# Kernel optimization log

Hardware: AMD Instinct MI355X
Metric: run time of the kernel (lower is better)

## Reference

```python
import jax, jax.numpy as jnp
import numpy as np

N_S, N_T, E = 50000, 50000, 600000
D_IN, D_H, D_OUT = 256, 128, 64


def setup_inputs() -> dict:
    key = jax.random.key(0)
    k1, k2, k3, k4, k5, k6 = jax.random.split(key, 6)
    edge_src = jax.random.randint(k1, (E,), 0, N_S, dtype=jnp.int32)
    edge_dst = jax.random.randint(k2, (E,), 0, N_T, dtype=jnp.int32)
    edge_index = jnp.stack([edge_src, edge_dst], axis=0)  # [2, E]
    x_s = jax.random.normal(k3, (N_S, D_IN), dtype=jnp.float32)
    x_t = jax.random.normal(k4, (N_T, D_IN), dtype=jnp.float32)
    W0 = jax.random.normal(k5, (D_IN, D_H), dtype=jnp.float32) * (1.0 / np.sqrt(D_IN))
    W1 = jax.random.normal(k6, (D_H, D_OUT), dtype=jnp.float32) * (1.0 / np.sqrt(D_H))
    return {"edge_index": edge_index, "x_s": x_s, "x_t": x_t, "W0": W0, "W1": W1}


def gcn_conv(x, src, dst, W):
    """PyG GCNConv, bias=False: D^{-1/2}(A+I)D^{-1/2} (x @ W)."""
    N = x.shape[0]
    h = x @ W  # [N, out]
    loops = jnp.arange(N, dtype=src.dtype)
    s = jnp.concatenate([src, loops])  # add self-loops
    d = jnp.concatenate([dst, loops])
    deg = jax.ops.segment_sum(jnp.ones_like(d, dtype=h.dtype), d, num_segments=N)
    dinv = jnp.where(deg > 0, jax.lax.rsqrt(deg), 0.0)
    norm = dinv[s] * dinv[d]  # [E+N]
    return jax.ops.segment_sum(h[s] * norm[:, None], d, num_segments=N)


def reference(edge_index, x_s, x_t, W0, W1):
    n_s = x_s.shape[0]
    src = edge_index[0]
    dst = edge_index[1] + n_s  # targets live in the x_t block
    acts = [jax.nn.relu, lambda v: v]
    Ws = [W0, W1]
    for W, act in zip(Ws, acts):
        x = jnp.concatenate([x_s, x_t], axis=0)
        x = act(gcn_conv(x, src, dst, W))
        x_s, x_t = x[:n_s], x[n_s:]
    return (x_s, x_t)
```

## Files before the change

### kernel.cpp

```cpp
#include <hip/hip_runtime.h>
#include <cstdint>
#include <cstddef>

typedef unsigned short u16;
typedef unsigned int   u32;
typedef __attribute__((ext_vector_type(8))) short bf16x8;
typedef __attribute__((ext_vector_type(4))) float f32x4;

#define D_IN  256
#define D_H   128
#define D_OUT 64

__device__ __forceinline__ float bf2f(u16 u){
  union { u32 i; float f; } v; v.i = ((u32)u) << 16; return v.f;
}
__device__ __forceinline__ u16 f2bf(float f){
  union { float f; u32 i; } v; v.f = f;
  u32 r = (v.i + 0x7fffu + ((v.i >> 16) & 1u)) >> 16;
  return (u16)r;
}

__global__ void k_wprep(const float* __restrict__ W0, const float* __restrict__ W1,
                        u16* __restrict__ W0t, u16* __restrict__ W1t,
                        int* __restrict__ deg, int n_t){
  int i = blockIdx.x * 256 + threadIdx.x;
  if (i < 128 * 256){
    int n = i >> 8, k = i & 255;
    W0t[i] = f2bf(W0[(size_t)k * 128 + n]);
  } else if (i < 128 * 256 + 64 * 128){
    int j = i - 128 * 256;
    int n = j >> 7, k = j & 127;
    W1t[j] = f2bf(W1[(size_t)k * 64 + n]);
  } else if (i - (128 * 256 + 64 * 128) < n_t){
    deg[i - (128 * 256 + 64 * 128)] = 0;
  }
}

__global__ __launch_bounds__(256) void k_off(const int* __restrict__ deg, int N,
                                             int* __restrict__ off, int* __restrict__ cursor,
                                             float* __restrict__ dinv){
  __shared__ int s[256];
  __shared__ int sbase[256];
  const int tid = threadIdx.x;
  const int bid = blockIdx.x;
  const int i   = bid * 256 + tid;
  int acc = 0;
  const int lim = bid * 256;
  for (int j = tid; j < lim; j += 256) acc += deg[j];
  sbase[tid] = acc;
  int v = (i < N) ? deg[i] : 0;
  s[tid] = v;
  __syncthreads();
  for (int o = 128; o > 0; o >>= 1){
    if (tid < o) sbase[tid] += sbase[tid + o];
    __syncthreads();
  }
  for (int o = 1; o < 256; o <<= 1){
    int tv = (tid >= o) ? s[tid - o] : 0;
    __syncthreads();
    s[tid] += tv;
    __syncthreads();
  }
  if (i < N){
    int excl = s[tid] - v + sbase[0];
    off[i] = excl;
    cursor[i] = excl;
    dinv[i] = rsqrtf((float)v + 1.0f);
  }
}

__global__ void k_fill(const int* __restrict__ src, const int* __restrict__ dst,
                       int E, int* __restrict__ cursor, int* __restrict__ csr){
  int e = blockIdx.x * 256 + threadIdx.x;
  if (e < E){
    int d = dst[e];
    int p = atomicAdd(&cursor[d], 1);
    csr[p] = src[e];
  }
}

__global__ __launch_bounds__(512, 4) void k_g1(
    const float* __restrict__ Xs, const float* __restrict__ Xt,
    const u16* __restrict__ W0t, int M, int n_s,
    const int* __restrict__ dst, int E, int* __restrict__ deg, int nbDeg,
    u16* __restrict__ out)
{
  __shared__ u16 Bs[128 * 256];
  const int t = threadIdx.x;

  if ((int)blockIdx.x < nbDeg){
    const int stride = nbDeg * 512;
    for (int e = blockIdx.x * 512 + t; e < E; e += stride)
      atomicAdd(&deg[dst[e]], 1);
    return;
  }

  const int wave = t >> 6, lane = t & 63;
  const int lm   = lane & 15, quad = lane >> 4;
  const int gw   = ((int)blockIdx.x - nbDeg) * 8 + wave;
  const int row  = gw * 16 + lm;

  int cr = (row < M) ? row : 0;
  const float* pa = ((cr < n_s) ? (Xs + (size_t)cr * D_IN)
                                : (Xt + (size_t)(cr - n_s) * D_IN)) + quad * 8;

  float4 a[8][2];
  a[0][0] = *(const float4*)(pa +  0); a[0][1] = *(const float4*)(pa +  4);
  a[1][0] = *(const float4*)(pa + 32); a[1][1] = *(const float4*)(pa + 36);

  {
    const int n = t >> 2;
    const int c = t & 3;
    const u16* wsrc = W0t + (size_t)n * 256 + c * 64;
    char* brow = (char*)Bs + n * 512;
    const int sw = (n & 15) << 4;
    #pragma unroll
    for (int j = 0; j < 8; j++){
      int off = (c * 128 + j * 16) ^ sw;
      *(int4*)(brow + off) = *(const int4*)(wsrc + j * 8);
    }
  }

  #pragma unroll
  for (int s = 2; s < 8; s++){
    a[s][0] = *(const float4*)(pa + s * 32);
    a[s][1] = *(const float4*)(pa + s * 32 + 4);
  }
  __builtin_amdgcn_sched_barrier(0);

  f32x4 acc[8];
  const f32x4 z = {0.f, 0.f, 0.f, 0.f};
  #pragma unroll
  for (int nf = 0; nf < 8; nf++) acc[nf] = z;

  __syncthreads();

  const char* bb = (const char*)Bs + lm * 512;
  const int lmx = lm << 4;

  #pragma unroll
  for (int kk = 0; kk < 8; kk++){
    bf16x8 af;
    {
      const float* fa = (const float*)&a[kk][0];
      u16 tmp[8];
      #pragma unroll
      for (int q = 0; q < 8; q++) tmp[q] = f2bf(fa[q]);
      af = *(const bf16x8*)tmp;
    }
    const int koff = (kk * 64 + quad * 16) ^ lmx;
    #pragma unroll
    for (int nf = 0; nf < 8; nf++){
      bf16x8 bf = *(const bf16x8*)(bb + nf * 8192 + koff);
      acc[nf] = __builtin_amdgcn_mfma_f32_16x16x32_bf16(af, bf, acc[nf], 0, 0, 0);
    }
  }

  __syncthreads();
  u16* wreg = Bs + wave * 2048;
  #pragma unroll
  for (int nf = 0; nf < 8; nf++){
    #pragma unroll
    for (int rr = 0; rr < 4; rr++){
      int rl = quad * 4 + rr;
      int c  = nf * 16 + lm;
      wreg[rl * 128 + (c ^ (quad << 5))] = f2bf(acc[nf][rr]);
    }
  }
  {
    const int g = lane >> 4, l = lane & 15;
    const int wrow0 = gw * 16;
    #pragma unroll
    for (int i = 0; i < 4; i++){
      int rl = i * 4 + g;
      int m  = wrow0 + rl;
      bf16x8 v = *(const bf16x8*)&wreg[rl * 128 + ((l ^ (i << 2)) << 3)];
      if (m < M) *(bf16x8*)(out + (size_t)m * D_H + l * 8) = v;
    }
  }
}

__device__ __forceinline__ void aggf_body(
    const int* __restrict__ off, const int* __restrict__ deg,
    const int* __restrict__ csr, const float* __restrict__ dinv,
    u16* __restrict__ h1, int n_s, int n_t, int w, int lane)
{
  if (w >= n_t) return;
  const int g = lane >> 4;
  const int c = lane & 15;
  int start = off[w];
  int n     = deg[w];

  float r[8], p[8];
  #pragma unroll
  for (int q = 0; q < 8; q++){ r[q] = 0.f; p[q] = 0.f; }

  int i = 0;
  for (; i + 8 <= n; i += 8){
    int sa = csr[start + i + g];
    int sb = csr[start + i + 4 + g];
    int4 da = *(const int4*)(h1 + (size_t)sa * D_H + c * 8);
    int4 db = *(const int4*)(h1 + (size_t)sb * D_H + c * 8);
    const u16* ha = (const u16*)&da;
    const u16* hb = (const u16*)&db;
    #pragma unroll
    for (int q = 0; q < 8; q++){
      float va = bf2f(ha[q]), vb = bf2f(hb[q]);
      r[q] += va + vb;
      p[q] += fmaxf(va, 0.f) + fmaxf(vb, 0.f);
    }
  }
  for (; i < n; i += 4){
    if (i + g < n){
      int sa = csr[start + i + g];
      int4 da = *(const int4*)(h1 + (size_t)sa * D_H + c * 8);
      const u16* ha = (const u16*)&da;
      #pragma unroll
      for (int q = 0; q < 8; q++){
        float va = bf2f(ha[q]);
        r[q] += va;
        p[q] += fmaxf(va, 0.f);
      }
    }
  }

  #pragma unroll
  for (int q = 0; q < 8; q++){
    r[q] += __shfl_xor(r[q], 16, 64);
    r[q] += __shfl_xor(r[q], 32, 64);
    p[q] += __shfl_xor(p[q], 16, 64);
    p[q] += __shfl_xor(p[q], 32, 64);
  }

  if (g == 0){
    float di  = dinv[w];
    float di2 = di * di;
    u16* selfp = h1 + (size_t)(n_s + w) * D_H + c * 8;
    int4 hs = *(const int4*)selfp;
    const u16* hh = (const u16*)&hs;
    u16 ob[8];
    #pragma unroll
    for (int q = 0; q < 8; q++){
      float zq = fmaxf(di * r[q] + di2 * bf2f(hh[q]), 0.f);
      float uq = di * p[q] + di2 * zq;
      ob[q] = f2bf(uq);
    }
    *(int4*)selfp = *(int4*)ob;
  }
}

__device__ __forceinline__ bf16x8 relu_bf(int4 v, bool relu){
  const u16* s = (const u16*)&v;
  u16 tmp[8];
  #pragma unroll
  for (int q = 0; q < 8; q++){
    u16 x = s[q];
    tmp[q] = (relu && (x & 0x8000u)) ? (u16)0 : x;
  }
  return *(const bf16x8*)tmp;
}

__device__ __forceinline__ void gemm2_body(
    const u16* __restrict__ h1, const u16* __restrict__ W1t,
    int gb, int base, int rowLim, int n_s, float* __restrict__ out,
    u16* Bs, float* Cb)
{
  const int t    = threadIdx.x;
  const int wave = t >> 6, lane = t & 63;
  const int lm   = lane & 15, quad = lane >> 4;
  const int gw   = gb * 8 + wave;
  const int row  = base + gw * 16 + lm;

  int cr = (row < rowLim) ? row : base;
  const bool relu = (cr < n_s);
  const u16* pa = h1 + (size_t)cr * D_H + quad * 8;

  int4 a[4];
  a[0] = *(const int4*)(pa);
  a[1] = *(const int4*)(pa + 32);

  {
    const int n = t >> 3;
    const int c = t & 7;
    const u16* wsrc = W1t + (size_t)n * 128 + c * 16;
    char* brow = (char*)Bs + n * 256;
    const int sw = (n & 15) << 4;
    #pragma unroll
    for (int j = 0; j < 2; j++){
      int off = (c * 32 + j * 16) ^ sw;
      *(int4*)(brow + off) = *(const int4*)(wsrc + j * 8);
    }
  }
  a[2] = *(const int4*)(pa + 64);
  a[3] = *(const int4*)(pa + 96);
  __builtin_amdgcn_sched_barrier(0);

  f32x4 acc[4];
  const f32x4 z = {0.f, 0.f, 0.f, 0.f};
  #pragma unroll
  for (int nf = 0; nf < 4; nf++) acc[nf] = z;

  __syncthreads();

  const char* bb = (const char*)Bs + lm * 256;
  const int lmx = lm << 4;

  #pragma unroll
  for (int kk = 0; kk < 4; kk++){
    bf16x8 af = relu_bf(a[kk], relu);
    const int koff = (kk * 64 + quad * 16) ^ lmx;
    #pragma unroll
    for (int nf = 0; nf < 4; nf++){
      bf16x8 bf = *(const bf16x8*)(bb + nf * 4096 + koff);
      acc[nf] = __builtin_amdgcn_mfma_f32_16x16x32_bf16(af, bf, acc[nf], 0, 0, 0);
    }
  }

  float* wreg = Cb + wave * 1024;
  #pragma unroll
  for (int nf = 0; nf < 4; nf++){
    #pragma unroll
    for (int rr = 0; rr < 4; rr++){
      int rl = quad * 4 + rr;
      int c  = nf * 16 + lm;
      wreg[rl * 64 + (c ^ (quad << 4))] = acc[nf][rr];
    }
  }
  {
    const int g = lane >> 4, l = lane & 15;
    const int wrow0 = base + gw * 16;
    #pragma unroll
    for (int i = 0; i < 4; i++){
      int rl = i * 4 + g;
      int m  = wrow0 + rl;
      float4 v = *(const float4*)&wreg[rl * 64 + ((l ^ (i << 2)) << 2)];
      if (m < rowLim) *(float4*)(out + (size_t)m * D_OUT + l * 4) = v;
    }
  }
}

__global__ __launch_bounds__(512, 4) void k_agg2s(
    const int* __restrict__ off, const int* __restrict__ deg,
    const int* __restrict__ csr, const float* __restrict__ dinv,
    u16* __restrict__ h1, int n_s, int n_t,
    const u16* __restrict__ W1t, float* __restrict__ out, int nbAgg)
{
  __shared__ u16  Bs[64 * 128];
  __shared__ float Cb[8 * 1024];
  if ((int)blockIdx.x < nbAgg){
    int w = blockIdx.x * 8 + (threadIdx.x >> 6);
    aggf_body(off, deg, csr, dinv, h1, n_s, n_t, w, threadIdx.x & 63);
  } else {
    gemm2_body(h1, W1t, (int)blockIdx.x - nbAgg, 0, n_s, n_s, out, Bs, Cb);
  }
}

__global__ __launch_bounds__(512, 4) void k_g2t(
    const u16* __restrict__ h1, const u16* __restrict__ W1t,
    int M, int n_s, float* __restrict__ out)
{
  __shared__ u16  Bs[64 * 128];
  __shared__ float Cb[8 * 1024];
  gemm2_body(h1, W1t, (int)blockIdx.x, n_s, M, n_s, out, Bs, Cb);
}

static inline size_t alup(size_t x){ return (x + 255) & ~(size_t)255; }

extern "C" void kernel_launch(void* const* d_in, const int* in_sizes, int n_in,
                              void* d_out, int out_size, void* d_ws, size_t ws_size,
                              hipStream_t stream)
{
  const int*   ei = (const int*)d_in[0];
  const float* xs = (const float*)d_in[1];
  const float* xt = (const float*)d_in[2];
  const float* W0 = (const float*)d_in[3];
  const float* W1 = (const float*)d_in[4];
  const int E   = in_sizes[0] / 2;
  const int n_s = in_sizes[1] / D_IN;
  const int n_t = in_sizes[2] / D_IN;
  const int M   = n_s + n_t;
  const int* src = ei;
  const int* dst = ei + E;

  char* p = (char*)d_ws;
  int*   deg    = (int*)p;    p += alup((size_t)n_t * 4);
  int*   off    = (int*)p;    p += alup((size_t)n_t * 4);
  int*   cursor = (int*)p;    p += alup((size_t)n_t * 4);
  float* dinv   = (float*)p;  p += alup((size_t)n_t * 4);
  int*   csr    = (int*)p;    p += alup((size_t)E * 4);
  u16*   W0t    = (u16*)p;    p += alup((size_t)D_H * D_IN * 2);
  u16*   W1t    = (u16*)p;    p += alup((size_t)D_OUT * D_H * 2);
  u16*   h1     = (u16*)p;    p += alup((size_t)M * D_H * 2);

  const int nb_t   = (n_t + 255) / 256;
  const int nbDeg  = 64;
  const int nbG1   = (M + 127) / 128;
  const int nbAgg  = (n_t + 7) / 8;
  const int nbG2s  = (n_s + 127) / 128;
  const int nbG2t  = (n_t + 127) / 128;

  const int wprep_n = 128*256 + 64*128 + n_t;
  k_wprep <<<(wprep_n + 255) / 256, 256, 0, stream>>>(W0, W1, W0t, W1t, deg, n_t);
  k_g1    <<<nbDeg + nbG1, 512, 0, stream>>>(xs, xt, W0t, M, n_s, dst, E, deg, nbDeg, h1);
  k_off   <<<nb_t, 256, 0, stream>>>(deg, n_t, off, cursor, dinv);
  k_fill  <<<(E + 255) / 256, 256, 0, stream>>>(src, dst, E, cursor, csr);
  k_agg2s <<<nbAgg + nbG2s, 512, 0, stream>>>(off, deg, csr, dinv, h1, n_s, n_t,
                                              W1t, (float*)d_out, nbAgg);
  k_g2t   <<<nbG2t, 512, 0, stream>>>(h1, W1t, M, n_s, (float*)d_out);
}
```

Measured before the change: 259.9 us.

## Issue all A-row loads via inline asm, memset degree array, double degree blocks

Result: slower. 267.4 us (+2.9%).

```diff
diff --git a/kernel.cpp b/kernel.cpp
--- a/kernel.cpp
+++ b/kernel.cpp
@@ -21,8 +21,7 @@
 }
 
 __global__ void k_wprep(const float* __restrict__ W0, const float* __restrict__ W1,
-                        u16* __restrict__ W0t, u16* __restrict__ W1t,
-                        int* __restrict__ deg, int n_t){
+                        u16* __restrict__ W0t, u16* __restrict__ W1t){
   int i = blockIdx.x * 256 + threadIdx.x;
   if (i < 128 * 256){
     int n = i >> 8, k = i & 255;
@@ -31,8 +30,6 @@
     int j = i - 128 * 256;
     int n = j >> 7, k = j & 127;
     W1t[j] = f2bf(W1[(size_t)k * 64 + n]);
-  } else if (i - (128 * 256 + 64 * 128) < n_t){
-    deg[i - (128 * 256 + 64 * 128)] = 0;
   }
 }
 
@@ -79,7 +76,7 @@
   }
 }
 
-__global__ __launch_bounds__(512, 4) void k_g1(
+__global__ __launch_bounds__(512) void k_g1(
     const float* __restrict__ Xs, const float* __restrict__ Xt,
     const u16* __restrict__ W0t, int M, int n_s,
     const int* __restrict__ dst, int E, int* __restrict__ deg, int nbDeg,
@@ -104,9 +101,23 @@
   const float* pa = ((cr < n_s) ? (Xs + (size_t)cr * D_IN)
                                 : (Xt + (size_t)(cr - n_s) * D_IN)) + quad * 8;
 
-  float4 a[8][2];
-  a[0][0] = *(const float4*)(pa +  0); a[0][1] = *(const float4*)(pa +  4);
-  a[1][0] = *(const float4*)(pa + 32); a[1][1] = *(const float4*)(pa + 36);
+  f32x4 A[16];
+  asm volatile("global_load_dwordx4 %0, %1, off offset:0"   : "=v"(A[ 0]) : "v"(pa));
+  asm volatile("global_load_dwordx4 %0, %1, off offset:16"  : "=v"(A[ 1]) : "v"(pa));
+  asm volatile("global_load_dwordx4 %0, %1, off offset:128" : "=v"(A[ 2]) : "v"(pa));
+  asm volatile("global_load_dwordx4 %0, %1, off offset:144" : "=v"(A[ 3]) : "v"(pa));
+  asm volatile("global_load_dwordx4 %0, %1, off offset:256" : "=v"(A[ 4]) : "v"(pa));
+  asm volatile("global_load_dwordx4 %0, %1, off offset:272" : "=v"(A[ 5]) : "v"(pa));
+  asm volatile("global_load_dwordx4 %0, %1, off offset:384" : "=v"(A[ 6]) : "v"(pa));
+  asm volatile("global_load_dwordx4 %0, %1, off offset:400" : "=v"(A[ 7]) : "v"(pa));
+  asm volatile("global_load_dwordx4 %0, %1, off offset:512" : "=v"(A[ 8]) : "v"(pa));
+  asm volatile("global_load_dwordx4 %0, %1, off offset:528" : "=v"(A[ 9]) : "v"(pa));
+  asm volatile("global_load_dwordx4 %0, %1, off offset:640" : "=v"(A[10]) : "v"(pa));
+  asm volatile("global_load_dwordx4 %0, %1, off offset:656" : "=v"(A[11]) : "v"(pa));
+  asm volatile("global_load_dwordx4 %0, %1, off offset:768" : "=v"(A[12]) : "v"(pa));
+  asm volatile("global_load_dwordx4 %0, %1, off offset:784" : "=v"(A[13]) : "v"(pa));
+  asm volatile("global_load_dwordx4 %0, %1, off offset:896" : "=v"(A[14]) : "v"(pa));
+  asm volatile("global_load_dwordx4 %0, %1, off offset:912" : "=v"(A[15]) : "v"(pa));
 
   {
     const int n = t >> 2;
@@ -121,19 +132,14 @@
     }
   }
 
-  #pragma unroll
-  for (int s = 2; s < 8; s++){
-    a[s][0] = *(const float4*)(pa + s * 32);
-    a[s][1] = *(const float4*)(pa + s * 32 + 4);
-  }
-  __builtin_amdgcn_sched_barrier(0);
-
   f32x4 acc[8];
   const f32x4 z = {0.f, 0.f, 0.f, 0.f};
   #pragma unroll
   for (int nf = 0; nf < 8; nf++) acc[nf] = z;
 
   __syncthreads();
+  asm volatile("s_waitcnt vmcnt(0)" ::: "memory");
+  __builtin_amdgcn_sched_barrier(0);
 
   const char* bb = (const char*)Bs + lm * 512;
   const int lmx = lm << 4;
@@ -142,10 +148,12 @@
   for (int kk = 0; kk < 8; kk++){
     bf16x8 af;
     {
-      const float* fa = (const float*)&a[kk][0];
+      f32x4 lo = A[2 * kk], hi = A[2 * kk + 1];
       u16 tmp[8];
-      #pragma unroll
-      for (int q = 0; q < 8; q++) tmp[q] = f2bf(fa[q]);
+      tmp[0] = f2bf(lo[0]); tmp[1] = f2bf(lo[1]);
+      tmp[2] = f2bf(lo[2]); tmp[3] = f2bf(lo[3]);
+      tmp[4] = f2bf(hi[0]); tmp[5] = f2bf(hi[1]);
+      tmp[6] = f2bf(hi[2]); tmp[7] = f2bf(hi[3]);
       af = *(const bf16x8*)tmp;
     }
     const int koff = (kk * 64 + quad * 16) ^ lmx;
@@ -393,14 +401,14 @@
   u16*   h1     = (u16*)p;    p += alup((size_t)M * D_H * 2);
 
   const int nb_t   = (n_t + 255) / 256;
-  const int nbDeg  = 64;
+  const int nbDeg  = 128;
   const int nbG1   = (M + 127) / 128;
   const int nbAgg  = (n_t + 7) / 8;
   const int nbG2s  = (n_s + 127) / 128;
   const int nbG2t  = (n_t + 127) / 128;
 
-  const int wprep_n = 128*256 + 64*128 + n_t;
-  k_wprep <<<(wprep_n + 255) / 256, 256, 0, stream>>>(W0, W1, W0t, W1t, deg, n_t);
+  hipMemsetAsync(deg, 0, (size_t)n_t * 4, stream);
+  k_wprep <<<160, 256, 0, stream>>>(W0, W1, W0t, W1t);
   k_g1    <<<nbDeg + nbG1, 512, 0, stream>>>(xs, xt, W0t, M, n_s, dst, E, deg, nbDeg, h1);
   k_off   <<<nb_t, 256, 0, stream>>>(deg, n_t, off, cursor, dinv);
   k_fill  <<<(E + 255) / 256, 256, 0, stream>>>(src, dst, E, cursor, csr);
```
